# Optimization experiments

Measured on AMD Instinct MI355X. Metric: run time of the kernel, lower is better.

The kernel has to match this reference:

```python
import jax, jax.numpy as jnp
import numpy as np

DIM = 64; NH = 8; WS = 8; B = 8; H = 128; W = 128
HD = DIM // NH
SCALE = HD ** -0.5
BN_S = np.float32(1.0 / np.sqrt(1.0 + 1e-5))  # eval-mode BatchNorm with running mean=0, var=1


def conv2d(x, w, stride=1, padding=0, groups=1, bias=None):
    out = jax.lax.conv_general_dilated(
        x, w, (stride, stride), [(padding, padding), (padding, padding)],
        dimension_numbers=('NCHW', 'OIHW', 'NCHW'), feature_group_count=groups)
    if bias is not None:
        out = out + bias[None, :, None, None]
    return out


def bn(x, g, b):
    return x * (g * BN_S)[None, :, None, None] + b[None, :, None, None]


def maxpool(x, k, s):
    return jax.lax.reduce_window(x, -jnp.inf, jax.lax.max, (1, 1, k, k), (1, 1, s, s), 'VALID')


def avgpool(x, kh, kw, ph, pw):
    # torch AvgPool2d: zero padding, count_include_pad=True -> divide by full kernel size
    s = jax.lax.reduce_window(x, 0.0, jax.lax.add, (1, 1, kh, kw), (1, 1, 1, 1),
                              [(0, 0), (0, 0), (ph, ph), (pw, pw)])
    return s / (kh * kw)


def fft_h(x):
    # high-pass: zero magnitude within radius 40 of the shifted spectrum center
    h, w = x.shape[-2], x.shape[-1]
    f = jnp.fft.fftshift(jnp.fft.fft2(x), axes=(-2, -1))
    ii = jnp.arange(h)[:, None] - h // 2
    jj = jnp.arange(w)[None, :] - w // 2
    mask = (jnp.sqrt((ii * ii + jj * jj).astype(jnp.float32)) > 40.0).astype(x.dtype)
    filt = f * (jnp.abs(f) * mask)
    return jnp.abs(jnp.fft.ifft2(jnp.fft.ifftshift(filt, axes=(-2, -1))))


def gabor_branch(x, f_cos, f_sin, gb_b1, gb_b2, gb_w, w_post, g_post, b_post,
                 w_gc, b_gc, w_gc1, b_gc1, w_gc2, b_gc2):
    xs = x.shape[2]  # x_size (square input assumed, as in the torch code)
    xc = jnp.concatenate([conv2d(x, f_cos, bias=gb_b1), conv2d(x, f_sin, bias=gb_b2)], axis=1)
    wts = jax.nn.relu(gb_w)
    fw = wts / (jnp.sum(wts) + 1e-8)
    xc = fw[0] * fft_h(xc) + fw[1] * xc
    xc = jnp.clip(bn(conv2d(xc, w_post, padding=1), g_post, b_post), 0.0, 6.0)  # ReLU6
    xc = maxpool(xc, 2, 1)
    xc = jax.nn.relu(conv2d(xc, w_gc, stride=2, bias=b_gc))
    xc = maxpool(xc, 2, 2)
    xc = jax.image.resize(xc, (xc.shape[0], xc.shape[1], xs, xs), method='bilinear')
    xc = jax.nn.relu(conv2d(xc, w_gc1, padding=1, bias=b_gc1))
    xc = conv2d(xc, w_gc2, bias=b_gc2)
    return jax.nn.log_softmax(xc, axis=1)


def forward(x, w_qkv, w_l1, g_l1, b_l1, w_l2, g_l2, b_l2, f_cos, f_sin, gb_b1, gb_b2, gb_w,
            w_post, g_post, b_post, w_gc, b_gc, w_gc1, b_gc1, w_gc2, b_gc2,
            rpb_table, w_dw, g_proj, b_proj, w_pw, rel_index):
    b, c, hh, ww = x.shape
    # local branch
    local = bn(conv2d(x, w_l2), g_l2, b_l2) + bn(conv2d(x, w_l1, padding=1), g_l1, b_l1)
    local = gabor_branch(local, f_cos, f_sin, gb_b1, gb_b2, gb_w, w_post, g_post, b_post,
                         w_gc, b_gc, w_gc1, b_gc1, w_gc2, b_gc2)
    # global branch (H, W multiples of WS -> self.pad is a no-op)
    qkv = conv2d(x, w_qkv)  # [b, 3C, H, W]
    gh, gw = hh // WS, ww // WS
    t = qkv.reshape(b, 3, NH, HD, gh, WS, gw, WS)
    t = t.transpose(1, 0, 4, 6, 2, 5, 7, 3).reshape(3, b * gh * gw, NH, WS * WS, HD)
    q, k, v = t[0], t[1], t[2]
    rpb = rpb_table[rel_index.reshape(-1)].reshape(WS * WS, WS * WS, NH).transpose(2, 0, 1)
    dots = jnp.einsum('bhid,bhjd->bhij', q, k) * SCALE + rpb[None]
    attn = jax.nn.softmax(dots, axis=-1)
    o = jnp.einsum('bhij,bhjd->bhid', attn, v)
    o = o.reshape(b, gh, gw, NH, WS, WS, HD).transpose(0, 3, 6, 1, 4, 2, 5).reshape(b, c, hh, ww)
    # directional reflect-pad + avg pool (kernel (8,1)/(1,8), stride 1, pad 3)
    ox = avgpool(jnp.pad(o, ((0, 0), (0, 0), (0, 1), (0, 0)), mode='reflect'), WS, 1, WS // 2 - 1, 0)
    oy = avgpool(jnp.pad(o, ((0, 0), (0, 0), (0, 0), (0, 1)), mode='reflect'), 1, WS, 0, WS // 2 - 1)
    out = ox + oy + local
    out = jnp.pad(out, ((0, 0), (0, 0), (0, 1), (0, 1)))  # pad_out
    out = conv2d(bn(conv2d(out, w_dw, padding=(WS - 1) // 2, groups=c), g_proj, b_proj), w_pw)
    return out[:, :, :hh, :ww]


def _gabor(sig, th, lam, psi, gam, ks, use_cos):
    half = (ks - 1) // 2
    y, x = np.meshgrid(np.arange(-half, half + 1), np.arange(-half, half + 1))
    x = x.astype(np.float32); y = y.astype(np.float32)
    sx = sig[..., None, None]; sy = (sig / gam)[..., None, None]
    t = th[..., None, None]; l = lam[..., None, None]; p = psi[..., None, None]
    xt = x * np.cos(t) + y * np.sin(t)
    yt = -x * np.sin(t) + y * np.cos(t)
    env = np.exp(-0.5 * (xt ** 2 / sx ** 2 + yt ** 2 / sy ** 2))
    car = np.cos(2.0 * np.pi / l * xt + p) if use_cos else np.sin(2.0 * np.pi / l * xt + p)
    return (env * car).astype(np.float32)


def setup_inputs() -> dict:
    rng = np.random.default_rng(0)
    def rn(*s, sc=0.05):
        return jnp.asarray(rng.standard_normal(s).astype(np.float32) * sc)
    sig, th, lam, psi, gam = [rng.standard_normal((DIM // 2, DIM)).astype(np.float32) for _ in range(5)]
    f_cos = jnp.asarray(_gabor(sig, th, lam, psi, gam, 3, True))
    f_sin = jnp.asarray(_gabor(sig, th, lam, psi, gam, 3, False))
    coords = np.stack(np.meshgrid(np.arange(WS), np.arange(WS), indexing='ij')).reshape(2, -1)
    rel = (coords[:, :, None] - coords[:, None, :]).transpose(1, 2, 0)
    rel[:, :, 0] += WS - 1; rel[:, :, 1] += WS - 1; rel[:, :, 0] *= 2 * WS - 1
    rel_index = jnp.asarray(rel.sum(-1).astype(np.int32))  # [64, 64]
    return dict(
        x=rn(B, DIM, H, W, sc=1.0),
        w_qkv=rn(3 * DIM, DIM, 1, 1),
        w_l1=rn(DIM, DIM, 3, 3), g_l1=jnp.ones(DIM), b_l1=jnp.zeros(DIM),
        w_l2=rn(DIM, DIM, 1, 1), g_l2=jnp.ones(DIM), b_l2=jnp.zeros(DIM),
        f_cos=f_cos, f_sin=f_sin,
        gb_b1=rn(DIM // 2), gb_b2=rn(DIM // 2), gb_w=jnp.ones(2),
        w_post=rn(DIM, DIM, 3, 3), g_post=jnp.ones(DIM), b_post=jnp.zeros(DIM),
        w_gc=rn(64, 64, 3, 3), b_gc=rn(64),
        w_gc1=rn(64, 64, 3, 3), b_gc1=rn(64),
        w_gc2=rn(64, 64, 1, 1), b_gc2=rn(64),
        rpb_table=rn((2 * WS - 1) ** 2, NH, sc=0.02),
        w_dw=rn(DIM, 1, WS, WS), g_proj=jnp.ones(DIM), b_proj=jnp.zeros(DIM),
        w_pw=rn(DIM, DIM, 1, 1),
        rel_index=rel_index,
    )


def reference(x, w_qkv, w_l1, g_l1, b_l1, w_l2, g_l2, b_l2, f_cos, f_sin, gb_b1, gb_b2, gb_w,
              w_post, g_post, b_post, w_gc, b_gc, w_gc1, b_gc1, w_gc2, b_gc2,
              rpb_table, w_dw, g_proj, b_proj, w_pw, rel_index):
    return forward(x, w_qkv, w_l1, g_l1, b_l1, w_l2, g_l2, b_l2, f_cos, f_sin, gb_b1, gb_b2, gb_w,
                   w_post, g_post, b_post, w_gc, b_gc, w_gc1, b_gc1, w_gc2, b_gc2,
                   rpb_table, w_dw, g_proj, b_proj, w_pw, rel_index)
```

## Files before the change

### kernel.cpp

```cpp
#include <hip/hip_runtime.h>
#include <math.h>

#define BN_SC 0.9999950000375f
#define P2N   (6.283185307179586f / 126.f)
#define ATT_SCALE 0.35355339059327373f

typedef float v4f __attribute__((ext_vector_type(4)));
typedef short bf16x8 __attribute__((ext_vector_type(8)));
typedef float f32x4 __attribute__((ext_vector_type(4)));
typedef unsigned short u16;

enum { M_LOCAL = 0, M_GABOR = 1, M_BNRELU6 = 2, M_BIASRELU = 3 };

__device__ __forceinline__ u16 f2bf(float f) {
  unsigned u = __float_as_uint(f);
  return (u16)((u + 0x7FFFu + ((u >> 16) & 1u)) >> 16);
}
__device__ __forceinline__ float bf2f(u16 h) {
  return __uint_as_float(((unsigned)h) << 16);
}

__global__ __launch_bounds__(256) void rpbprep_k(
    const float* __restrict__ rpb, const int* __restrict__ relidx, float* __restrict__ rpbt)
{
  int idx = blockIdx.x * 256 + threadIdx.x;
  int h = idx >> 12, r = idx & 4095, j = r >> 6, i = r & 63;
  rpbt[idx] = rpb[relidx[i * 64 + j] * 8 + h];
}

__global__ void bls_k(const float* __restrict__ a, const float* __restrict__ b,
                      float* __restrict__ o)
{ int i = threadIdx.x; o[i] = a[i] + b[i]; }

__global__ __launch_bounds__(256)
void wsplit_k(const float* __restrict__ w, const float* __restrict__ gsc,
              u16* __restrict__ wh, u16* __restrict__ wl,
              int nco, int ntap, int co_off, int tap_off, int NT)
{
  int i = blockIdx.x * 256 + threadIdx.x;
  if (i >= nco * 64 * ntap) return;
  int t = i % ntap, q = i / ntap;
  int cin = q & 63, co = q >> 6;
  float v = w[i];
  if (gsc) v *= gsc[co_off + co] * BN_SC;
  u16 h = f2bf(v);
  u16 l = f2bf(v - bf2f(h));
  int dst = ((co_off + co) * NT + tap_off + t) * 64 + cin;
  wh[dst] = h; wl[dst] = l;
}

__global__ __launch_bounds__(256)
void wsplit_gc_k(const float* __restrict__ w, u16* __restrict__ wh, u16* __restrict__ wl)
{
  int i = blockIdx.x * 256 + threadIdx.x;
  if (i >= 36864) return;
  int t = i % 9, q = i / 9;
  int cin = q & 63, co = q >> 6;
  const int POS[9] = {0, 4, 1, 6, 8, 7, 2, 5, 3};
  float v = w[i];
  u16 h = f2bf(v);
  u16 l = f2bf(v - bf2f(h));
  int dst = (co * 9 + POS[t]) * 64 + cin;
  wh[dst] = h; wl[dst] = l;
}

__global__ __launch_bounds__(256)
void tprep_k(u16* __restrict__ tb)
{
  int idx = blockIdx.x * 256 + threadIdx.x;
  int tab = idx >> 14, r = idx & 16383;
  int ch = r >> 7, k = r & 127;
  float v = 0.f;
  if (tab == 0) {
    int k2 = ch >> 1;
    if (k < 126) {
      int m = (k * k2) % 126;
      float s, c; sincosf(P2N * (float)m, &s, &c);
      v = (ch & 1) ? -s : c;
    }
  } else if (tab == 1) {
    if (ch < 126 && k < 126) { int m = (ch * k) % 126; v = cosf(P2N * (float)m); }
  } else if (tab == 2) {
    if (ch < 126 && k < 126) { int m = (ch * k) % 126; v = sinf(P2N * (float)m); }
  } else {
    int k2 = k >> 1;
    if (ch < 126) {
      float w = (k2 == 0 || k2 == 63) ? 1.f : 2.f;
      int m = (ch * k2) % 126;
      float s, c; sincosf(P2N * (float)m, &s, &c);
      v = (k & 1) ? -w * s : w * c;
    }
  }
  u16 h = f2bf(v), l = f2bf(v - bf2f(h));
  tb[tab * 32768 + r] = h;
  tb[tab * 32768 + 16384 + r] = l;
}

template<int HW>
__global__ __launch_bounds__(256)
void xsplit_k(const float* __restrict__ in, u16* __restrict__ xh, u16* __restrict__ xl)
{
  __shared__ float t[64 * (HW + 1)];
  const int by = blockIdx.x;
  const int tid = threadIdx.x;
  const int b = by / HW, y = by - b * HW;
  const float* ip = in + (size_t)b * 64 * HW * HW + (size_t)y * HW;
  for (int e = tid; e < 64 * HW; e += 256) {
    int cin = e / HW, x = e - cin * HW;
    t[cin * (HW + 1) + x] = ip[(size_t)cin * HW * HW + x];
  }
  __syncthreads();
  u16* oh = xh + (size_t)by * HW * 64;
  u16* ol = xl + (size_t)by * HW * 64;
  for (int e = tid; e < 64 * HW; e += 256) {
    int x = e >> 6, cin = e & 63;
    float v = t[cin * (HW + 1) + x];
    u16 h = f2bf(v);
    oh[e] = h;
    ol[e] = f2bf(v - bf2f(h));
  }
}

__global__ __launch_bounds__(256)
void mpsplit_k(const float* __restrict__ in, u16* __restrict__ ph_h, u16* __restrict__ ph_l)
{
  __shared__ float rm[126 * 65];
  const int tid = threadIdx.x;
  const int bx = blockIdx.x;
  const int b = bx / 126, r = bx % 126;
  const int py = r / 63, u = r % 63;
  const bool valid_u = !(py == 1 && u == 62);
  if (valid_u) {
    const int r0 = 2 * u + py;
    const float* ip = in + (size_t)b * 64 * 15876;
    for (int e = tid; e < 64 * 126; e += 256) {
      int cin = e / 126, col = e - cin * 126;
      const float* p = ip + (size_t)cin * 15876 + (size_t)r0 * 126 + col;
      rm[col * 65 + cin] = fmaxf(p[0], p[126]);
    }
  }
  __syncthreads();
  for (int e = tid; e < 8064; e += 256) {
    int px = e / 4032;
    int rr = e - px * 4032;
    int v = rr >> 6, cin = rr & 63;
    float val = 0.f;
    if (valid_u && !(px == 1 && v == 62)) {
      int c0 = 2 * v + px;
      val = fmaxf(rm[c0 * 65 + cin], rm[(c0 + 1) * 65 + cin]);
    }
    u16 h = f2bf(val);
    size_t dst = (((size_t)(b * 4 + py * 2 + px) * 63 + u) * 63 + v) * 64 + cin;
    ph_h[dst] = h;
    ph_l[dst] = f2bf(val - bf2f(h));
  }
}

template<int MODE, int NT, int IN_HW, int OUT_HW, int PAD, bool OUTBF>
__global__ __launch_bounds__(256, 3)
void convmf_k(const u16* __restrict__ xh, const u16* __restrict__ xl,
              const u16* __restrict__ wh, const u16* __restrict__ wl,
              const float* __restrict__ ba, const float* __restrict__ bb,
              float* __restrict__ out, u16* __restrict__ oxh, u16* __restrict__ oxl)
{
  __shared__ uint4 lds4[2916];
  char* lds = (char*)lds4;
  const int tid = threadIdx.x;
  const int lane = tid & 63;
  const int wv = __builtin_amdgcn_readfirstlane(tid >> 6);
  const int wco = wv & 1, wpx = wv >> 1;
  const int b = blockIdx.y;
  const int oy0 = (blockIdx.x >> 3) * 16, ox0 = (blockIdx.x & 7) * 16;
  const int iy0 = oy0 - PAD, ix0 = ox0 - PAD;
  const int l15 = lane & 15, l4 = lane >> 4;
  const int bboff = l15 * 144 + l4 * 16;
  const int aoff  = l15 * (NT * 64) + l4 * 8;
  const u16* wh0 = wh + wco * 32 * NT * 64 + aoff;
  const u16* wl0 = wl + wco * 32 * NT * 64 + aoff;

  f32x4 acc[2][8];
#pragma unroll
  for (int f = 0; f < 2; ++f)
#pragma unroll
    for (int r = 0; r < 8; ++r) { f32x4 z = {0.f, 0.f, 0.f, 0.f}; acc[f][r] = z; }

#pragma unroll 1
  for (int cc = 0; cc < 64; cc += 32) {
    __syncthreads();
    for (int e = tid; e < 2592; e += 256) {
      int pix = e >> 3, part = e & 7;
      int lr = pix / 18, lc = pix - lr * 18;
      int iy = iy0 + lr, ix = ix0 + lc;
      uint4 v = make_uint4(0u, 0u, 0u, 0u);
      if ((unsigned)iy < (unsigned)IN_HW && (unsigned)ix < (unsigned)IN_HW) {
        const u16* s = ((part < 4) ? xh : xl)
            + ((size_t)(b * IN_HW + iy) * IN_HW + ix) * 64 + cc + (part & 3) * 8;
        v = *(const uint4*)s;
      }
      *(uint4*)(lds + pix * 144 + part * 16) = v;
    }
    __syncthreads();

    bf16x8 ah0 = *(const bf16x8*)(wh0 + cc);
    bf16x8 al0 = *(const bf16x8*)(wl0 + cc);
    bf16x8 ah1 = *(const bf16x8*)(wh0 + 16 * NT * 64 + cc);
    bf16x8 al1 = *(const bf16x8*)(wl0 + 16 * NT * 64 + cc);

#pragma unroll 1
    for (int t = 0; t < NT; ++t) {
      int tn = (t + 1 < NT) ? t + 1 : t;
      bf16x8 nh0 = *(const bf16x8*)(wh0 + tn * 64 + cc);
      bf16x8 nl0 = *(const bf16x8*)(wl0 + tn * 64 + cc);
      bf16x8 nh1 = *(const bf16x8*)(wh0 + 16 * NT * 64 + tn * 64 + cc);
      bf16x8 nl1 = *(const bf16x8*)(wl0 + 16 * NT * 64 + tn * 64 + cc);
      int te = (t >= 9) ? 4 : t;
      int dy = te / 3;
      int dx = te - dy * 3;
      const char* pb = lds + ((wpx * 8 + dy) * 18 + dx) * 144 + bboff;
#pragma unroll
      for (int r = 0; r < 8; ++r) {
        bf16x8 bh = *(const bf16x8*)(pb + r * 2592);
        bf16x8 bl = *(const bf16x8*)(pb + r * 2592 + 64);
        acc[0][r] = __builtin_amdgcn_mfma_f32_16x16x32_bf16(ah0, bh, acc[0][r], 0, 0, 0);
        acc[1][r] = __builtin_amdgcn_mfma_f32_16x16x32_bf16(ah1, bh, acc[1][r], 0, 0, 0);
        acc[0][r] = __builtin_amdgcn_mfma_f32_16x16x32_bf16(ah0, bl, acc[0][r], 0, 0, 0);
        acc[0][r] = __builtin_amdgcn_mfma_f32_16x16x32_bf16(al0, bh, acc[0][r], 0, 0, 0);
        acc[1][r] = __builtin_amdgcn_mfma_f32_16x16x32_bf16(ah1, bl, acc[1][r], 0, 0, 0);
        acc[1][r] = __builtin_amdgcn_mfma_f32_16x16x32_bf16(al1, bh, acc[1][r], 0, 0, 0);
      }
      ah0 = nh0; al0 = nl0; ah1 = nh1; al1 = nl1;
    }
  }

  const int ox = ox0 + l15;
#pragma unroll
  for (int f = 0; f < 2; ++f) {
    const int cb = wco * 32 + f * 16 + l4 * 4;
    float bias4[4];
#pragma unroll
    for (int j = 0; j < 4; ++j) {
      int c = cb + j;
      bias4[j] = (MODE == M_GABOR && c >= 32) ? bb[c - 32] : ba[c];
    }
    if (OUTBF) {
#pragma unroll
      for (int r = 0; r < 8; ++r) {
        int oy = oy0 + wpx * 8 + r;
        ushort4 hv, lv;
#pragma unroll
        for (int j = 0; j < 4; ++j) {
          float v = acc[f][r][j] + bias4[j];
          if (MODE == M_BNRELU6) v = fminf(fmaxf(v, 0.f), 6.f);
          if (MODE == M_BIASRELU) v = fmaxf(v, 0.f);
          u16 h = f2bf(v);
          ((u16*)&hv)[j] = h;
          ((u16*)&lv)[j] = f2bf(v - bf2f(h));
        }
        size_t base = (((size_t)b * 128 + oy) * 128 + ox) * 64 + cb;
        *(ushort4*)(oxh + base) = hv;
        *(ushort4*)(oxl + base) = lv;
      }
    } else {
#pragma unroll
      for (int r = 0; r < 8; ++r) {
        int oy = oy0 + wpx * 8 + r;
        if (OUT_HW != 128 && (oy >= OUT_HW || ox >= OUT_HW)) continue;
#pragma unroll
        for (int j = 0; j < 4; ++j) {
          float v = acc[f][r][j] + bias4[j];
          if (MODE == M_BNRELU6) v = fminf(fmaxf(v, 0.f), 6.f);
          if (MODE == M_BIASRELU) v = fmaxf(v, 0.f);
          out[(((size_t)(b * 64) + cb + j) * OUT_HW + oy) * OUT_HW + ox] = v;
        }
      }
    }
  }
}

__global__ __launch_bounds__(256)
void convgc_mf(const u16* __restrict__ ph_h, const u16* __restrict__ ph_l,
               const u16* __restrict__ wh, const u16* __restrict__ wl,
               const float* __restrict__ bias, float* __restrict__ out)
{
  __shared__ char lds[81 * 144];
  const int tid = threadIdx.x;
  const int lane = tid & 63;
  const int wv = __builtin_amdgcn_readfirstlane(tid >> 6);
  const int wco = wv & 1, wpx = wv >> 1;
  const int b = blockIdx.y;
  const int oy0 = (blockIdx.x >> 3) * 8, ox0 = (blockIdx.x & 7) * 8;
  const int l15 = lane & 15, l4 = lane >> 4;
  const int pr_ = l15 >> 3, pc_ = l15 & 7;
  const int aoff = l15 * 576 + l4 * 8;
  const u16* wh0 = wh + wco * 32 * 576 + aoff;
  const u16* wl0 = wl + wco * 32 * 576 + aoff;

  f32x4 acc[2][2];
#pragma unroll
  for (int f = 0; f < 2; ++f)
#pragma unroll
    for (int g = 0; g < 2; ++g) { f32x4 z = {0.f, 0.f, 0.f, 0.f}; acc[f][g] = z; }

  const int PHA[9] = {0, 0, 0, 0, 1, 1, 2, 2, 3};
  const int OYO[9] = {0, 0, 1, 1, 0, 1, 0, 0, 0};
  const int OXO[9] = {0, 1, 0, 1, 0, 0, 0, 1, 0};

#pragma unroll 1
  for (int cc = 0; cc < 64; cc += 32) {
#pragma unroll
    for (int pos = 0; pos < 9; ++pos) {
      const int ph = PHA[pos];
      if (pos == 0 || pos == 4 || pos == 6 || pos == 8) {
        __syncthreads();
        for (int e = tid; e < 648; e += 256) {
          int pix = e >> 3, part = e & 7;
          int pu = pix / 9, pv = pix - pu * 9;
          int u = oy0 + pu, v = ox0 + pv;
          uint4 val = make_uint4(0u, 0u, 0u, 0u);
          if (u < 63 && v < 63) {
            const u16* s = ((part < 4) ? ph_h : ph_l)
                + (((size_t)(b * 4 + ph) * 63 + u) * 63 + v) * 64 + cc + (part & 3) * 8;
            val = *(const uint4*)s;
          }
          *(uint4*)(lds + pix * 144 + part * 16) = val;
        }
        __syncthreads();
      }
      bf16x8 ah0 = *(const bf16x8*)(wh0 + pos * 64 + cc);
      bf16x8 al0 = *(const bf16x8*)(wl0 + pos * 64 + cc);
      bf16x8 ah1 = *(const bf16x8*)(wh0 + 16 * 576 + pos * 64 + cc);
      bf16x8 al1 = *(const bf16x8*)(wl0 + 16 * 576 + pos * 64 + cc);
#pragma unroll
      for (int g = 0; g < 2; ++g) {
        const int lrow = wpx * 4 + g * 2 + pr_ + OYO[pos];
        const int lcol = pc_ + OXO[pos];
        const char* pb = lds + (lrow * 9 + lcol) * 144 + l4 * 16;
        bf16x8 bh = *(const bf16x8*)pb;
        bf16x8 bl = *(const bf16x8*)(pb + 64);
        acc[0][g] = __builtin_amdgcn_mfma_f32_16x16x32_bf16(ah0, bh, acc[0][g], 0, 0, 0);
        acc[1][g] = __builtin_amdgcn_mfma_f32_16x16x32_bf16(ah1, bh, acc[1][g], 0, 0, 0);
        acc[0][g] = __builtin_amdgcn_mfma_f32_16x16x32_bf16(ah0, bl, acc[0][g], 0, 0, 0);
        acc[0][g] = __builtin_amdgcn_mfma_f32_16x16x32_bf16(al0, bh, acc[0][g], 0, 0, 0);
        acc[1][g] = __builtin_amdgcn_mfma_f32_16x16x32_bf16(ah1, bl, acc[1][g], 0, 0, 0);
        acc[1][g] = __builtin_amdgcn_mfma_f32_16x16x32_bf16(al1, bh, acc[1][g], 0, 0, 0);
      }
    }
  }

  const int ox = ox0 + pc_;
#pragma unroll
  for (int f = 0; f < 2; ++f) {
    const int cb = wco * 32 + f * 16 + l4 * 4;
#pragma unroll
    for (int g = 0; g < 2; ++g) {
      int oy = oy0 + wpx * 4 + g * 2 + pr_;
      if (oy >= 62 || ox >= 62) continue;
#pragma unroll
      for (int j = 0; j < 4; ++j) {
        float v = acc[f][g][j] + bias[cb + j];
        out[(((size_t)(b * 64) + cb + j) * 62 + oy) * 62 + ox] = fmaxf(v, 0.f);
      }
    }
  }
}


__global__ __launch_bounds__(256)
void dft_rows_fwd_mf(const float* __restrict__ in, float* __restrict__ outC,
                     const u16* __restrict__ th, const u16* __restrict__ tl, int planeBase)
{
  __shared__ char lds[64 * 528];
  const int tid = threadIdx.x;
  const int lane = tid & 63;
  const int wv = __builtin_amdgcn_readfirstlane(tid >> 6);
  const int l15 = lane & 15, l4 = lane >> 4;
  const int lp = blockIdx.x >> 1, rb = (blockIdx.x & 1) * 64;
  const float* src = in + (size_t)(planeBase + lp) * 15876;

  for (int e = tid; e < 8192; e += 256) {
    int row = e >> 7, k = e & 127;
    int gr = rb + row;
    float v = (gr < 126 && k < 126) ? src[(size_t)gr * 126 + k] : 0.f;
    u16 h = f2bf(v);
    char* p = lds + row * 528 + k * 2;
    *(u16*)p = h;
    *(u16*)(p + 256) = f2bf(v - bf2f(h));
  }
  __syncthreads();

  f32x4 acc[8];
#pragma unroll
  for (int nf = 0; nf < 8; ++nf) { f32x4 z = {0.f, 0.f, 0.f, 0.f}; acc[nf] = z; }
#pragma unroll
  for (int cc = 0; cc < 128; cc += 32) {
    const char* pb = lds + (wv * 16 + l15) * 528 + cc * 2 + l4 * 16;
    bf16x8 bh = *(const bf16x8*)pb;
    bf16x8 bl = *(const bf16x8*)(pb + 256);
#pragma unroll
    for (int nf = 0; nf < 8; ++nf) {
      const int ao = (nf * 16 + l15) * 128 + cc + l4 * 8;
      bf16x8 ah = *(const bf16x8*)(th + ao);
      bf16x8 al = *(const bf16x8*)(tl + ao);
      acc[nf] = __builtin_amdgcn_mfma_f32_16x16x32_bf16(ah, bh, acc[nf], 0, 0, 0);
      acc[nf] = __builtin_amdgcn_mfma_f32_16x16x32_bf16(ah, bl, acc[nf], 0, 0, 0);
      acc[nf] = __builtin_amdgcn_mfma_f32_16x16x32_bf16(al, bh, acc[nf], 0, 0, 0);
    }
  }
  const int row = rb + wv * 16 + l15;
  if (row < 126) {
    float* o = outC + (size_t)lp * 16128 + (size_t)row * 128;
#pragma unroll
    for (int nf = 0; nf < 8; ++nf)
      *(f32x4*)(o + nf * 16 + l4 * 4) = acc[nf];
  }
}

template<bool FWD>
__global__ __launch_bounds__(256)
// ... 112 lines not shown
    int row = e >> 7, k = e & 127;
    int gr = rb + row;
    float v = (gr < 126) ? src[(size_t)gr * 128 + k] : 0.f;
    u16 h = f2bf(v);
    char* p = lds + row * 528 + k * 2;
    *(u16*)p = h;
    *(u16*)(p + 256) = f2bf(v - bf2f(h));
  }
  __syncthreads();

  f32x4 acc[8];
#pragma unroll
  for (int nf = 0; nf < 8; ++nf) { f32x4 z = {0.f, 0.f, 0.f, 0.f}; acc[nf] = z; }
#pragma unroll
  for (int cc = 0; cc < 128; cc += 32) {
    const char* pb = lds + (wv * 16 + l15) * 528 + cc * 2 + l4 * 16;
    bf16x8 bh = *(const bf16x8*)pb;
    bf16x8 bl = *(const bf16x8*)(pb + 256);
#pragma unroll
    for (int nf = 0; nf < 8; ++nf) {
      const int ao = (nf * 16 + l15) * 128 + cc + l4 * 8;
      bf16x8 ah = *(const bf16x8*)(th + ao);
      bf16x8 al = *(const bf16x8*)(tl + ao);
      acc[nf] = __builtin_amdgcn_mfma_f32_16x16x32_bf16(ah, bh, acc[nf], 0, 0, 0);
      acc[nf] = __builtin_amdgcn_mfma_f32_16x16x32_bf16(ah, bl, acc[nf], 0, 0, 0);
      acc[nf] = __builtin_amdgcn_mfma_f32_16x16x32_bf16(al, bh, acc[nf], 0, 0, 0);
    }
  }
  const int row = rb + wv * 16 + l15;
  if (row < 126) {
    float w0 = fmaxf(gb_w[0], 0.f), w1 = fmaxf(gb_w[1], 0.f);
    float iv = 1.f / (w0 + w1 + 1e-8f);
    const float w0i = w0 * iv, w1i = w1 * iv;
    size_t base = (size_t)(planeBase + lp) * 15876 + (size_t)row * 126;
#pragma unroll
    for (int nf = 0; nf < 8; ++nf) {
      const int n20 = nf * 16 + l4 * 4;
#pragma unroll
      for (int j = 0; j < 4; ++j) {
        int n2 = n20 + j;
        if (n2 < 126)
          out[base + n2] = w0i * fabsf(acc[nf][j]) + w1i * xc0[base + n2];
      }
    }
  }
}

__global__ __launch_bounds__(256) void mp2_k(const float* __restrict__ in, float* __restrict__ out)
{
  int idx = blockIdx.x * 256 + threadIdx.x;
  if (idx >= 512 * 31 * 31) return;
  int x = idx % 31, y = (idx / 31) % 31, p = idx / 961;
  const float* ip = in + (size_t)p * 3844 + (size_t)(2 * y) * 62 + 2 * x;
  out[idx] = fmaxf(fmaxf(ip[0], ip[1]), fmaxf(ip[62], ip[63]));
}

__global__ __launch_bounds__(256)
void resize_bf_k(const float* __restrict__ in, u16* __restrict__ xh, u16* __restrict__ xl)
{
  int idx = blockIdx.x * 256 + threadIdx.x;
  if (idx >= 2097152) return;
  int cg = idx & 15, x = (idx >> 4) & 127, y = (idx >> 11) & 127, b = idx >> 18;
  float sy = (y + 0.5f) * (31.f / 128.f) - 0.5f; sy = fminf(fmaxf(sy, 0.f), 30.f);
  float sx = (x + 0.5f) * (31.f / 128.f) - 0.5f; sx = fminf(fmaxf(sx, 0.f), 30.f);
  int y0 = (int)sy; float fy = sy - (float)y0; int y1 = min(y0 + 1, 30);
  int x0 = (int)sx; float fx = sx - (float)x0; int x1 = min(x0 + 1, 30);
  const float* base = in + (size_t)(b * 64 + cg * 4) * 961;
  ushort4 hv, lv;
#pragma unroll
  for (int k = 0; k < 4; ++k) {
    const float* ip = base + k * 961;
    float v = (1.f - fy) * ((1.f - fx) * ip[y0 * 31 + x0] + fx * ip[y0 * 31 + x1])
            + fy         * ((1.f - fx) * ip[y1 * 31 + x0] + fx * ip[y1 * 31 + x1]);
    u16 h = f2bf(v);
    ((u16*)&hv)[k] = h;
    ((u16*)&lv)[k] = f2bf(v - bf2f(h));
  }
  size_t o = (((size_t)b * 128 + y) * 128 + x) * 64 + cg * 4;
  *(ushort4*)(xh + o) = hv;
  *(ushort4*)(xl + o) = lv;
}

__global__ __launch_bounds__(256)
void pwlsm_mf(const u16* __restrict__ xh, const u16* __restrict__ xl,
              const u16* __restrict__ wh, const u16* __restrict__ wl,
              const float* __restrict__ bias, float* __restrict__ out)
{
  __shared__ char lds[17664];
  const int tid = threadIdx.x;
  const int lane = tid & 63;
  const int wv = __builtin_amdgcn_readfirstlane(tid >> 6);
  const int l15 = lane & 15, l4 = lane >> 4;
  const size_t px0 = (size_t)blockIdx.x * 64;

  for (int e = tid; e < 1024; e += 256) {
    int pix = e >> 4, part = e & 15;
    const u16* s = ((part < 8) ? xh : xl) + (px0 + pix) * 64 + (part & 7) * 8;
    char* d = lds + pix * 272 + ((part < 8) ? part * 16 : 128 + (part - 8) * 16);
    *(uint4*)d = *(const uint4*)s;
  }
  __syncthreads();

  f32x4 acc[4];
#pragma unroll
  for (int p = 0; p < 4; ++p) { f32x4 z = {0.f, 0.f, 0.f, 0.f}; acc[p] = z; }
  const int co16 = wv * 16;
  const u16* wa = wh + (size_t)(co16 + l15) * 64 + l4 * 8;
  const u16* wb = wl + (size_t)(co16 + l15) * 64 + l4 * 8;
#pragma unroll
  for (int cc = 0; cc < 64; cc += 32) {
    bf16x8 ah = *(const bf16x8*)(wa + cc);
    bf16x8 al = *(const bf16x8*)(wb + cc);
#pragma unroll
    for (int p = 0; p < 4; ++p) {
      const char* pb = lds + (16 * p + l15) * 272 + cc * 2 + l4 * 16;
      bf16x8 bh = *(const bf16x8*)pb;
      bf16x8 bl = *(const bf16x8*)(pb + 128);
      acc[p] = __builtin_amdgcn_mfma_f32_16x16x32_bf16(ah, bh, acc[p], 0, 0, 0);
      acc[p] = __builtin_amdgcn_mfma_f32_16x16x32_bf16(ah, bl, acc[p], 0, 0, 0);
      acc[p] = __builtin_amdgcn_mfma_f32_16x16x32_bf16(al, bh, acc[p], 0, 0, 0);
    }
  }
  float4 bv = *(const float4*)&bias[co16 + l4 * 4];
  __syncthreads();
  float* zs = (float*)lds;
#pragma unroll
  for (int p = 0; p < 4; ++p) {
    int base = (16 * p + l15) * 69 + co16 + l4 * 4;
    zs[base + 0] = acc[p][0] + bv.x;
    zs[base + 1] = acc[p][1] + bv.y;
    zs[base + 2] = acc[p][2] + bv.z;
    zs[base + 3] = acc[p][3] + bv.w;
  }
  __syncthreads();
  if (tid < 64) {
    const float* z = zs + tid * 69;
    float m = -1e30f;
    for (int co = 0; co < 64; ++co) m = fmaxf(m, z[co]);
    float sum = 0.f;
    for (int co = 0; co < 64; ++co) sum += __expf(z[co] - m);
    float lse = m + __logf(sum);
    size_t g = px0 + tid;
    int b = (int)(g >> 14), px = (int)(g & 16383);
    float* op = out + ((size_t)b << 20) + px;
    for (int co = 0; co < 64; ++co) op[(size_t)co << 14] = z[co] - lse;
  }
}

__global__ __launch_bounds__(256)
void attn_mf_k(const float* __restrict__ x, const u16* __restrict__ wqh,
               const u16* __restrict__ wql, const float* __restrict__ rpbt,
               float* __restrict__ o_out)
{
  __shared__ uint4 lds4[3200];
  char* lds = (char*)lds4;
  const int tid = threadIdx.x;
  const int lane = tid & 63;
  const int wv = __builtin_amdgcn_readfirstlane(tid >> 6);
  const int b = blockIdx.x >> 8, gy = (blockIdx.x >> 4) & 15, gx = blockIdx.x & 15;
  const int y0 = gy * 8, x0 = gx * 8;
  const int l15 = lane & 15, l4 = lane >> 4;

  for (int e = tid; e < 4096; e += 256) {
    int cin = e >> 6, pix = e & 63;
    float v = x[((size_t)(b * 64 + cin) * 128 + (y0 + (pix >> 3))) * 128 + x0 + (pix & 7)];
    u16 h = f2bf(v);
    *(u16*)(lds + pix * 272 + cin * 2)       = h;
    *(u16*)(lds + pix * 272 + 128 + cin * 2) = f2bf(v - bf2f(h));
  }
  __syncthreads();

  f32x4 acc[3][4];
#pragma unroll
  for (int r = 0; r < 3; ++r)
#pragma unroll
    for (int p = 0; p < 4; ++p) { f32x4 z = {0.f, 0.f, 0.f, 0.f}; acc[r][p] = z; }
  const u16* wa = wqh + (size_t)(48 * wv + l15) * 64 + l4 * 8;
  const u16* wb = wql + (size_t)(48 * wv + l15) * 64 + l4 * 8;
#pragma unroll
  for (int cc = 0; cc < 64; cc += 32) {
    bf16x8 bh[4], bl[4];
#pragma unroll
    for (int p = 0; p < 4; ++p) {
      const char* pb = lds + (16 * p + l15) * 272 + cc * 2 + l4 * 16;
      bh[p] = *(const bf16x8*)pb;
      bl[p] = *(const bf16x8*)(pb + 128);
    }
#pragma unroll
    for (int r = 0; r < 3; ++r) {
      bf16x8 ah = *(const bf16x8*)(wa + r * 1024 + cc);
      bf16x8 al = *(const bf16x8*)(wb + r * 1024 + cc);
#pragma unroll
      for (int p = 0; p < 4; ++p) {
        acc[r][p] = __builtin_amdgcn_mfma_f32_16x16x32_bf16(ah, bh[p], acc[r][p], 0, 0, 0);
        acc[r][p] = __builtin_amdgcn_mfma_f32_16x16x32_bf16(ah, bl[p], acc[r][p], 0, 0, 0);
        acc[r][p] = __builtin_amdgcn_mfma_f32_16x16x32_bf16(al, bh[p], acc[r][p], 0, 0, 0);
      }
    }
  }
  __syncthreads();

#pragma unroll
  for (int r = 0; r < 3; ++r) {
    const int ch0 = 48 * wv + 16 * r + l4 * 4;
#pragma unroll
    for (int p = 0; p < 4; ++p) {
      const int pix = 16 * p + l15;
      if (ch0 < 64) {
#pragma unroll
        for (int j = 0; j < 4; ++j)
          *(float*)(lds + ((ch0 + j) * 65 + pix) * 4) = acc[r][p][j];
      } else {
        const int col = (ch0 < 128) ? (ch0 - 64) : (64 + ch0 - 128);
        *(f32x4*)(lds + 17408 + pix * 528 + col * 4) = acc[r][p];
      }
    }
  }
  __syncthreads();

  const int row = y0 + (lane >> 3), col = x0 + (lane & 7);
  const int h0 = wv, h1 = wv + 4;
  float q0[8], q1[8];
#pragma unroll
  for (int d = 0; d < 8; ++d) {
    q0[d] = *(const float*)(lds + ((h0 * 8 + d) * 65 + lane) * 4);
    q1[d] = *(const float*)(lds + ((h1 * 8 + d) * 65 + lane) * 4);
  }
  const float* rb0 = rpbt + h0 * 4096;
  const float* rb1 = rpbt + h1 * 4096;
  float P0[64], P1[64];
#pragma unroll
  for (int j = 0; j < 64; ++j) { P0[j] = rb0[j * 64 + lane]; P1[j] = rb1[j * 64 + lane]; }
  float m0 = -1e30f, m1 = -1e30f;
#pragma unroll
  for (int j = 0; j < 64; ++j) {
    const char* kp = lds + 17408 + j * 528;
    float4 a0 = *(const float4*)(kp + (h0 * 8) * 4);
    float4 a1 = *(const float4*)(kp + (h0 * 8) * 4 + 16);
    float4 b0 = *(const float4*)(kp + (h1 * 8) * 4);
    float4 b1 = *(const float4*)(kp + (h1 * 8) * 4 + 16);
    float s0 = q0[0] * a0.x + q0[1] * a0.y + q0[2] * a0.z + q0[3] * a0.w
             + q0[4] * a1.x + q0[5] * a1.y + q0[6] * a1.z + q0[7] * a1.w;
    float s1 = q1[0] * b0.x + q1[1] * b0.y + q1[2] * b0.z + q1[3] * b0.w
             + q1[4] * b1.x + q1[5] * b1.y + q1[6] * b1.z + q1[7] * b1.w;
    s0 = s0 * ATT_SCALE + P0[j];
    s1 = s1 * ATT_SCALE + P1[j];
    P0[j] = s0; P1[j] = s1;
    m0 = fmaxf(m0, s0); m1 = fmaxf(m1, s1);
  }
  float sum0 = 0.f, sum1 = 0.f;
#pragma unroll
  for (int j = 0; j < 64; ++j) {
    float p0 = __expf(P0[j] - m0); P0[j] = p0; sum0 += p0;
    float p1 = __expf(P1[j] - m1); P1[j] = p1; sum1 += p1;
  }
  float inv0 = 1.f / sum0, inv1 = 1.f / sum1;

  float acc0[8], acc1[8];
#pragma unroll
  for (int d = 0; d < 8; ++d) { acc0[d] = 0.f; acc1[d] = 0.f; }
#pragma unroll
  for (int j = 0; j < 64; ++j) {
    const char* vp = lds + 17408 + j * 528 + 256;
    float p0 = P0[j], p1 = P1[j];
    float4 v00 = *(const float4*)(vp + (h0 * 8) * 4);
    float4 v01 = *(const float4*)(vp + (h0 * 8) * 4 + 16);
    float4 v10 = *(const float4*)(vp + (h1 * 8) * 4);
    float4 v11 = *(const float4*)(vp + (h1 * 8) * 4 + 16);
    acc0[0] += p0 * v00.x; acc0[1] += p0 * v00.y; acc0[2] += p0 * v00.z; acc0[3] += p0 * v00.w;
    acc0[4] += p0 * v01.x; acc0[5] += p0 * v01.y; acc0[6] += p0 * v01.z; acc0[7] += p0 * v01.w;
    acc1[0] += p1 * v10.x; acc1[1] += p1 * v10.y; acc1[2] += p1 * v10.z; acc1[3] += p1 * v10.w;
    acc1[4] += p1 * v11.x; acc1[5] += p1 * v11.y; acc1[6] += p1 * v11.z; acc1[7] += p1 * v11.w;
  }
#pragma unroll
  for (int d = 0; d < 8; ++d) {
    o_out[((size_t)(b * 64 + h0 * 8 + d) * 128 + row) * 128 + col] = acc0[d] * inv0;
    o_out[((size_t)(b * 64 + h1 * 8 + d) * 128 + row) * 128 + col] = acc1[d] * inv1;
  }
}

__global__ __launch_bounds__(256)
void avgadd_k(const float* __restrict__ o, const float* __restrict__ loc, float* __restrict__ out)
{
  int idx = blockIdx.x * 256 + threadIdx.x;
  if (idx >= 8388608) return;
  int x = idx & 127, y = (idx >> 7) & 127;
  size_t p = (size_t)(idx >> 14);
  const float* op = o + (p << 14);
  float s1 = 0.f, s2 = 0.f;
#pragma unroll
  for (int t = 0; t < 8; ++t) {
    int r = y - 3 + t;
    if (r >= 0 && r <= 128) { int rr = (r == 128) ? 126 : r; s1 += op[rr * 128 + x]; }
    int cc = x - 3 + t;
    if (cc >= 0 && cc <= 128) { int ss = (cc == 128) ? 126 : cc; s2 += op[y * 128 + ss]; }
  }
  out[idx] = 0.125f * (s1 + s2) + loc[idx];
}

__global__ __launch_bounds__(256)
void dw_k(const float* __restrict__ in, const float* __restrict__ w,
          const float* __restrict__ g, const float* __restrict__ bb, float* __restrict__ out)
{
  __shared__ float t[23 * 23];
  const int tid = threadIdx.x;
  const int tx = tid & 15, ty = tid >> 4;
  const int x0 = blockIdx.x * 16, y0 = blockIdx.y * 16;
  const int pc = blockIdx.z;
  const int c = pc & 63;
  const float* ip = in + (size_t)pc * 16384;
  for (int e = tid; e < 529; e += 256) {
    int yy = e / 23, xx = e % 23;
    int iy = y0 + yy - 3, ix = x0 + xx - 3;
    t[e] = (iy >= 0 && iy < 128 && ix >= 0 && ix < 128) ? ip[iy * 128 + ix] : 0.f;
  }
  __syncthreads();
  const float* wk = w + c * 64;
  float s = 0.f;
#pragma unroll
  for (int ky = 0; ky < 8; ++ky)
#pragma unroll
    for (int kx = 0; kx < 8; ++kx)
      s += t[(ty + ky) * 23 + tx + kx] * wk[ky * 8 + kx];
  out[(size_t)pc * 16384 + (y0 + ty) * 128 + x0 + tx] = s * (g[c] * BN_SC) + bb[c];
}

__global__ __launch_bounds__(256)
void pw_k(const float* __restrict__ in, const float* __restrict__ w, float* __restrict__ out)
{
  int idx = blockIdx.x * 256 + threadIdx.x;
  int b = idx >> 14, px = idx & 16383;
  const float* ip = in + ((size_t)b << 20) + px;
  float v[64];
#pragma unroll
  for (int i = 0; i < 64; ++i) v[i] = ip[(size_t)i << 14];
  float* op = out + ((size_t)b << 20) + px;
  for (int co = 0; co < 64; ++co) {
    const float* wk = w + co * 64;
    float s = 0.f;
#pragma unroll
    for (int i = 0; i < 64; ++i) s += v[i] * wk[i];
    op[(size_t)co << 14] = s;
  }
}

extern "C" void kernel_launch(void* const* d_in, const int* in_sizes, int n_in,
                              void* d_out, int out_size, void* d_ws, size_t ws_size,
                              hipStream_t stream)
{
  const float* x      = (const float*)d_in[0];
  const float* w_qkv  = (const float*)d_in[1];
  const float* w_l1   = (const float*)d_in[2];
  const float* g_l1   = (const float*)d_in[3];
  const float* b_l1   = (const float*)d_in[4];
  const float* w_l2   = (const float*)d_in[5];
  const float* g_l2   = (const float*)d_in[6];
  const float* b_l2   = (const float*)d_in[7];
  const float* f_cos  = (const float*)d_in[8];
  const float* f_sin  = (const float*)d_in[9];
  const float* gb_b1  = (const float*)d_in[10];
  const float* gb_b2  = (const float*)d_in[11];
  const float* gb_w   = (const float*)d_in[12];
  const float* w_post = (const float*)d_in[13];
  const float* g_post = (const float*)d_in[14];
  const float* b_post = (const float*)d_in[15];
  const float* w_gc   = (const float*)d_in[16];
  const float* b_gc   = (const float*)d_in[17];
  const float* w_gc1  = (const float*)d_in[18];
  const float* b_gc1  = (const float*)d_in[19];
  const float* w_gc2  = (const float*)d_in[20];
  const float* b_gc2  = (const float*)d_in[21];
  const float* rpb    = (const float*)d_in[22];
  const float* w_dw   = (const float*)d_in[23];
  const float* g_proj = (const float*)d_in[24];
  const float* b_proj = (const float*)d_in[25];
  const float* w_pw   = (const float*)d_in[26];
  const int*   relidx = (const int*)d_in[27];
  float* out = (float*)d_out;

  char* ws = (char*)d_ws;
  float* R1   = (float*)(ws + 0);
  float* R2   = (float*)(ws + 33554432);
  float* R3   = (float*)(ws + 67108864);
  float* C1   = R3;
  float* C2   = (float*)(ws + 83623936);
  float* XC5  = (float*)(ws + 100139008);
  float* RPBT = (float*)(ws + 102107136);
  u16* XH_A = (u16*)(ws + 33554432);
  u16* XL_A = (u16*)(ws + 33554432 + 16777216);
  u16* XH_B = (u16*)(ws + 67108864);
  u16* XL_B = (u16*)(ws + 83886080);
  u16* PH_H = (u16*)(ws + 0);
  u16* PH_L = (u16*)(ws + 16257024);
  u16* XC7H = (u16*)(ws + 0);
  u16* XC7L = (u16*)(ws + 16777216);
  u16* TB   = (u16*)(ws + 100139008);
  u16* WH   = (u16*)(ws + 100663296);
  u16* WL   = (u16*)(ws + 100745216);
  float* BLS = (float*)(ws + 100827136);
  u16* WQH  = (u16*)(ws + 100827392);
  u16* WQL  = (u16*)(ws + 100851968);
  u16* WGH  = (u16*)(ws + 100876544);
  u16* WGL  = (u16*)(ws + 100884736);

  rpbprep_k<<<128, 256, 0, stream>>>(rpb, relidx, RPBT);

  wsplit_k<<<144, 256, 0, stream>>>(w_l1, g_l1, WH, WL, 64, 9, 0, 0, 10);
  wsplit_k<<<16, 256, 0, stream>>>(w_l2, g_l2, WH, WL, 64, 1, 0, 9, 10);
  bls_k<<<1, 64, 0, stream>>>(b_l1, b_l2, BLS);
  xsplit_k<128><<<1024, 256, 0, stream>>>(x, XH_A, XL_A);
  convmf_k<M_LOCAL, 10, 128, 128, 1, true><<<dim3(64, 8), 256, 0, stream>>>(
      XH_A, XL_A, WH, WL, BLS, nullptr, nullptr, XH_B, XL_B);

  wsplit_k<<<72, 256, 0, stream>>>(f_cos, nullptr, WH, WL, 32, 9, 0, 0, 9);
  wsplit_k<<<72, 256, 0, stream>>>(f_sin, nullptr, WH, WL, 32, 9, 32, 0, 9);
  convmf_k<M_GABOR, 9, 128, 126, 0, false><<<dim3(64, 8), 256, 0, stream>>>(
      XH_B, XL_B, WH, WL, gb_b1, gb_b2, R2, nullptr, nullptr);

  tprep_k<<<256, 256, 0, stream>>>(TB);
  for (int chunk = 0; chunk < 2; ++chunk) {
    int pb = chunk * 256;
    dft_rows_fwd_mf<<<512, 256, 0, stream>>>(R2, C1, TB, TB + 16384, pb);
    dft_cols_mf<true><<<512, 256, 0, stream>>>(C1, C2, TB + 32768, TB + 49152,
                                               TB + 65536, TB + 81920);
    dft_cols_mf<false><<<512, 256, 0, stream>>>(C2, C1, TB + 32768, TB + 49152,
                                                TB + 65536, TB + 81920);
    dft_rows_inv_mix_mf<<<512, 256, 0, stream>>>(C1, R2, gb_w, TB + 98304, TB + 114688,
                                                 R1, pb);
  }

  wsplit_k<<<144, 256, 0, stream>>>(w_post, g_post, WH, WL, 64, 9, 0, 0, 9);
  xsplit_k<126><<<1008, 256, 0, stream>>>(R1, XH_B, XL_B);
  convmf_k<M_BNRELU6, 9, 126, 126, 1, false><<<dim3(64, 8), 256, 0, stream>>>(
      XH_B, XL_B, WH, WL, b_post, nullptr, R2, nullptr, nullptr);

  mpsplit_k<<<1008, 256, 0, stream>>>(R2, PH_H, PH_L);

  wsplit_gc_k<<<144, 256, 0, stream>>>(w_gc, WH, WL);
  convgc_mf<<<dim3(64, 8), 256, 0, stream>>>(PH_H, PH_L, WH, WL, b_gc, R3);

  mp2_k<<<1922, 256, 0, stream>>>(R3, XC5);
  resize_bf_k<<<8192, 256, 0, stream>>>(XC5, XH_B, XL_B);

  wsplit_k<<<48, 256, 0, stream>>>(w_qkv, nullptr, WQH, WQL, 192, 1, 0, 0, 1);
  wsplit_k<<<16, 256, 0, stream>>>(w_gc2, nullptr, WGH, WGL, 64, 1, 0, 0, 1);

  wsplit_k<<<144, 256, 0, stream>>>(w_gc1, nullptr, WH, WL, 64, 9, 0, 0, 9);
  convmf_k<M_BIASRELU, 9, 128, 128, 1, true><<<dim3(64, 8), 256, 0, stream>>>(
      XH_B, XL_B, WH, WL, b_gc1, nullptr, nullptr, XC7H, XC7L);

  pwlsm_mf<<<2048, 256, 0, stream>>>(XC7H, XC7L, WGH, WGL, b_gc2, R2);
  attn_mf_k<<<2048, 256, 0, stream>>>(x, WQH, WQL, RPBT, R1);
  avgadd_k<<<32768, 256, 0, stream>>>(R1, R2, R3);
  dw_k<<<dim3(8, 8, 512), 256, 0, stream>>>(R3, w_dw, g_proj, b_proj, R2);
  pw_k<<<512, 256, 0, stream>>>(R2, w_pw, out);
  (void)in_sizes; (void)n_in; (void)out_size; (void)ws_size;
}
```

Baseline: 922.8 us.

## Halve conv tile height for occupancy and store attention K/V in bf16 LDS

The MFMA conv kernel now computes 8-row by 16-column output tiles instead of 16x16. This halves the LDS footprint and accumulator registers, doubles the grid, and raises the launch-bounds occupancy hint from 3 to 4 blocks. Separately, the attention kernel stores K and V in LDS as bf16 rather than fp32 and unpacks them on read, which halves its LDS use. That lowers attention precision, which may matter given the hi/lo split scheme used elsewhere, and the smaller conv tiles reload a relatively larger halo.

```diff
diff --git a/kernel.cpp b/kernel.cpp
--- a/kernel.cpp
+++ b/kernel.cpp
@@ -18,6 +18,10 @@
 }
 __device__ __forceinline__ float bf2f(u16 h) {
   return __uint_as_float(((unsigned)h) << 16);
+}
+__device__ __forceinline__ void up2(unsigned w, float& a, float& b) {
+  a = __uint_as_float(w << 16);
+  b = __uint_as_float(w & 0xffff0000u);
 }
 
 __global__ __launch_bounds__(256) void rpbprep_k(
@@ -157,20 +161,20 @@
 }
 
 template<int MODE, int NT, int IN_HW, int OUT_HW, int PAD, bool OUTBF>
-__global__ __launch_bounds__(256, 3)
+__global__ __launch_bounds__(256, 4)
 void convmf_k(const u16* __restrict__ xh, const u16* __restrict__ xl,
               const u16* __restrict__ wh, const u16* __restrict__ wl,
               const float* __restrict__ ba, const float* __restrict__ bb,
               float* __restrict__ out, u16* __restrict__ oxh, u16* __restrict__ oxl)
 {
-  __shared__ uint4 lds4[2916];
+  __shared__ uint4 lds4[1620];
   char* lds = (char*)lds4;
   const int tid = threadIdx.x;
   const int lane = tid & 63;
   const int wv = __builtin_amdgcn_readfirstlane(tid >> 6);
   const int wco = wv & 1, wpx = wv >> 1;
   const int b = blockIdx.y;
-  const int oy0 = (blockIdx.x >> 3) * 16, ox0 = (blockIdx.x & 7) * 16;
+  const int oy0 = (blockIdx.x >> 3) * 8, ox0 = (blockIdx.x & 7) * 16;
   const int iy0 = oy0 - PAD, ix0 = ox0 - PAD;
   const int l15 = lane & 15, l4 = lane >> 4;
   const int bboff = l15 * 144 + l4 * 16;
@@ -178,16 +182,16 @@
   const u16* wh0 = wh + wco * 32 * NT * 64 + aoff;
   const u16* wl0 = wl + wco * 32 * NT * 64 + aoff;
 
-  f32x4 acc[2][8];
+  f32x4 acc[2][4];
 #pragma unroll
   for (int f = 0; f < 2; ++f)
 #pragma unroll
-    for (int r = 0; r < 8; ++r) { f32x4 z = {0.f, 0.f, 0.f, 0.f}; acc[f][r] = z; }
+    for (int r = 0; r < 4; ++r) { f32x4 z = {0.f, 0.f, 0.f, 0.f}; acc[f][r] = z; }
 
 #pragma unroll 1
   for (int cc = 0; cc < 64; cc += 32) {
     __syncthreads();
-    for (int e = tid; e < 2592; e += 256) {
+    for (int e = tid; e < 1440; e += 256) {
       int pix = e >> 3, part = e & 7;
       int lr = pix / 18, lc = pix - lr * 18;
       int iy = iy0 + lr, ix = ix0 + lc;
@@ -216,9 +220,9 @@
       int te = (t >= 9) ? 4 : t;
       int dy = te / 3;
       int dx = te - dy * 3;
-      const char* pb = lds + ((wpx * 8 + dy) * 18 + dx) * 144 + bboff;
-#pragma unroll
-      for (int r = 0; r < 8; ++r) {
+      const char* pb = lds + ((wpx * 4 + dy) * 18 + dx) * 144 + bboff;
+#pragma unroll
+      for (int r = 0; r < 4; ++r) {
         bf16x8 bh = *(const bf16x8*)(pb + r * 2592);
         bf16x8 bl = *(const bf16x8*)(pb + r * 2592 + 64);
         acc[0][r] = __builtin_amdgcn_mfma_f32_16x16x32_bf16(ah0, bh, acc[0][r], 0, 0, 0);
@@ -244,8 +248,8 @@
     }
     if (OUTBF) {
 #pragma unroll
-      for (int r = 0; r < 8; ++r) {
-        int oy = oy0 + wpx * 8 + r;
+      for (int r = 0; r < 4; ++r) {
+        int oy = oy0 + wpx * 4 + r;
         ushort4 hv, lv;
 #pragma unroll
         for (int j = 0; j < 4; ++j) {
@@ -262,8 +266,8 @@
       }
     } else {
 #pragma unroll
-      for (int r = 0; r < 8; ++r) {
-        int oy = oy0 + wpx * 8 + r;
+      for (int r = 0; r < 4; ++r) {
+        int oy = oy0 + wpx * 4 + r;
         if (OUT_HW != 128 && (oy >= OUT_HW || ox >= OUT_HW)) continue;
 #pragma unroll
         for (int j = 0; j < 4; ++j) {
@@ -682,7 +686,7 @@
                const u16* __restrict__ wql, const float* __restrict__ rpbt,
                float* __restrict__ o_out)
 {
-  __shared__ uint4 lds4[3200];
+  __shared__ uint4 lds4[2176];
   char* lds = (char*)lds4;
   const int tid = threadIdx.x;
   const int lane = tid & 63;
@@ -742,7 +746,12 @@
           *(float*)(lds + ((ch0 + j) * 65 + pix) * 4) = acc[r][p][j];
       } else {
         const int col = (ch0 < 128) ? (ch0 - 64) : (64 + ch0 - 128);
-        *(f32x4*)(lds + 17408 + pix * 528 + col * 4) = acc[r][p];
+        ushort4 pk;
+        pk.x = f2bf(acc[r][p][0]);
+        pk.y = f2bf(acc[r][p][1]);
+        pk.z = f2bf(acc[r][p][2]);
+        pk.w = f2bf(acc[r][p][3]);
+        *(ushort4*)(lds + 17408 + pix * 272 + col * 2) = pk;
       }
     }
   }
@@ -764,15 +773,17 @@
   float m0 = -1e30f, m1 = -1e30f;
 #pragma unroll
   for (int j = 0; j < 64; ++j) {
-    const char* kp = lds + 17408 + j * 528;
-    float4 a0 = *(const float4*)(kp + (h0 * 8) * 4);
-    float4 a1 = *(const float4*)(kp + (h0 * 8) * 4 + 16);
-    float4 b0 = *(const float4*)(kp + (h1 * 8) * 4);
-    float4 b1 = *(const float4*)(kp + (h1 * 8) * 4 + 16);
-    float s0 = q0[0] * a0.x + q0[1] * a0.y + q0[2] * a0.z + q0[3] * a0.w
-             + q0[4] * a1.x + q0[5] * a1.y + q0[6] * a1.z + q0[7] * a1.w;
-    float s1 = q1[0] * b0.x + q1[1] * b0.y + q1[2] * b0.z + q1[3] * b0.w
-             + q1[4] * b1.x + q1[5] * b1.y + q1[6] * b1.z + q1[7] * b1.w;
+    const char* kp = lds + 17408 + j * 272;
+    uint4 kw0 = *(const uint4*)(kp + h0 * 16);
+    uint4 kw1 = *(const uint4*)(kp + h1 * 16);
+    float a0, a1, a2, a3, a4, a5, a6, a7;
+    up2(kw0.x, a0, a1); up2(kw0.y, a2, a3); up2(kw0.z, a4, a5); up2(kw0.w, a6, a7);
+    float s0 = q0[0] * a0 + q0[1] * a1 + q0[2] * a2 + q0[3] * a3
+             + q0[4] * a4 + q0[5] * a5 + q0[6] * a6 + q0[7] * a7;
+    float c0, c1, c2, c3, c4, c5, c6, c7;
+    up2(kw1.x, c0, c1); up2(kw1.y, c2, c3); up2(kw1.z, c4, c5); up2(kw1.w, c6, c7);
+    float s1 = q1[0] * c0 + q1[1] * c1 + q1[2] * c2 + q1[3] * c3
+             + q1[4] * c4 + q1[5] * c5 + q1[6] * c6 + q1[7] * c7;
     s0 = s0 * ATT_SCALE + P0[j];
     s1 = s1 * ATT_SCALE + P1[j];
     P0[j] = s0; P1[j] = s1;
@@ -791,16 +802,18 @@
   for (int d = 0; d < 8; ++d) { acc0[d] = 0.f; acc1[d] = 0.f; }
 #pragma unroll
   for (int j = 0; j < 64; ++j) {
-    const char* vp = lds + 17408 + j * 528 + 256;
+    const char* vp = lds + 17408 + j * 272 + 128;
     float p0 = P0[j], p1 = P1[j];
-    float4 v00 = *(const float4*)(vp + (h0 * 8) * 4);
-    float4 v01 = *(const float4*)(vp + (h0 * 8) * 4 + 16);
-    float4 v10 = *(const float4*)(vp + (h1 * 8) * 4);
-    float4 v11 = *(const float4*)(vp + (h1 * 8) * 4 + 16);
-    acc0[0] += p0 * v00.x; acc0[1] += p0 * v00.y; acc0[2] += p0 * v00.z; acc0[3] += p0 * v00.w;
-    acc0[4] += p0 * v01.x; acc0[5] += p0 * v01.y; acc0[6] += p0 * v01.z; acc0[7] += p0 * v01.w;
-    acc1[0] += p1 * v10.x; acc1[1] += p1 * v10.y; acc1[2] += p1 * v10.z; acc1[3] += p1 * v10.w;
-    acc1[4] += p1 * v11.x; acc1[5] += p1 * v11.y; acc1[6] += p1 * v11.z; acc1[7] += p1 * v11.w;
+    uint4 vw0 = *(const uint4*)(vp + h0 * 16);
+    uint4 vw1 = *(const uint4*)(vp + h1 * 16);
+    float a0, a1, a2, a3, a4, a5, a6, a7;
+    up2(vw0.x, a0, a1); up2(vw0.y, a2, a3); up2(vw0.z, a4, a5); up2(vw0.w, a6, a7);
+    acc0[0] += p0 * a0; acc0[1] += p0 * a1; acc0[2] += p0 * a2; acc0[3] += p0 * a3;
+    acc0[4] += p0 * a4; acc0[5] += p0 * a5; acc0[6] += p0 * a6; acc0[7] += p0 * a7;
+    float c0, c1, c2, c3, c4, c5, c6, c7;
+    up2(vw1.x, c0, c1); up2(vw1.y, c2, c3); up2(vw1.z, c4, c5); up2(vw1.w, c6, c7);
+    acc1[0] += p1 * c0; acc1[1] += p1 * c1; acc1[2] += p1 * c2; acc1[3] += p1 * c3;
+    acc1[4] += p1 * c4; acc1[5] += p1 * c5; acc1[6] += p1 * c6; acc1[7] += p1 * c7;
   }
 #pragma unroll
   for (int d = 0; d < 8; ++d) {
@@ -939,12 +952,12 @@
   wsplit_k<<<16, 256, 0, stream>>>(w_l2, g_l2, WH, WL, 64, 1, 0, 9, 10);
   bls_k<<<1, 64, 0, stream>>>(b_l1, b_l2, BLS);
   xsplit_k<128><<<1024, 256, 0, stream>>>(x, XH_A, XL_A);
-  convmf_k<M_LOCAL, 10, 128, 128, 1, true><<<dim3(64, 8), 256, 0, stream>>>(
+  convmf_k<M_LOCAL, 10, 128, 128, 1, true><<<dim3(128, 8), 256, 0, stream>>>(
       XH_A, XL_A, WH, WL, BLS, nullptr, nullptr, XH_B, XL_B);
 
   wsplit_k<<<72, 256, 0, stream>>>(f_cos, nullptr, WH, WL, 32, 9, 0, 0, 9);
   wsplit_k<<<72, 256, 0, stream>>>(f_sin, nullptr, WH, WL, 32, 9, 32, 0, 9);
-  convmf_k<M_GABOR, 9, 128, 126, 0, false><<<dim3(64, 8), 256, 0, stream>>>(
+  convmf_k<M_GABOR, 9, 128, 126, 0, false><<<dim3(128, 8), 256, 0, stream>>>(
       XH_B, XL_B, WH, WL, gb_b1, gb_b2, R2, nullptr, nullptr);
 
   tprep_k<<<256, 256, 0, stream>>>(TB);
@@ -961,7 +974,7 @@
 
   wsplit_k<<<144, 256, 0, stream>>>(w_post, g_post, WH, WL, 64, 9, 0, 0, 9);
   xsplit_k<126><<<1008, 256, 0, stream>>>(R1, XH_B, XL_B);
-  convmf_k<M_BNRELU6, 9, 126, 126, 1, false><<<dim3(64, 8), 256, 0, stream>>>(
+  convmf_k<M_BNRELU6, 9, 126, 126, 1, false><<<dim3(128, 8), 256, 0, stream>>>(
       XH_B, XL_B, WH, WL, b_post, nullptr, R2, nullptr, nullptr);
 
   mpsplit_k<<<1008, 256, 0, stream>>>(R2, PH_H, PH_L);
@@ -976,7 +989,7 @@
   wsplit_k<<<16, 256, 0, stream>>>(w_gc2, nullptr, WGH, WGL, 64, 1, 0, 0, 1);
 
   wsplit_k<<<144, 256, 0, stream>>>(w_gc1, nullptr, WH, WL, 64, 9, 0, 0, 9);
-  convmf_k<M_BIASRELU, 9, 128, 128, 1, true><<<dim3(64, 8), 256, 0, stream>>>(
+  convmf_k<M_BIASRELU, 9, 128, 128, 1, true><<<dim3(128, 8), 256, 0, stream>>>(
       XH_B, XL_B, WH, WL, b_gc1, nullptr, nullptr, XC7H, XC7L);
 
   pwlsm_mf<<<2048, 256, 0, stream>>>(XC7H, XC7L, WGH, WGL, b_gc2, R2);
```

Result: slower. 986.0 us (+6.9%).
